# Performance work log

Measured on AMD Instinct MI355X. Metric: run time of the kernel, lower is better.

Reference implementation:

```python
import jax, jax.numpy as jnp
import numpy as np

B, S, D, H = 2, 4096, 256, 4
DH = D // H  # head dim = 64


def setup_inputs() -> dict:
    key = jax.random.key(0)
    ks = jax.random.split(key, 7)
    scale = 1.0 / np.sqrt(D)
    return {
        "x": jax.random.normal(ks[0], (B, S, D), dtype=jnp.float32),
        "Wq": jax.random.normal(ks[1], (D, D), dtype=jnp.float32) * scale,
        "bq": jax.random.normal(ks[2], (D,), dtype=jnp.float32) * scale,
        "Wk": jax.random.normal(ks[3], (D, D), dtype=jnp.float32) * scale,
        "bk": jax.random.normal(ks[4], (D,), dtype=jnp.float32) * scale,
        "Wv": jax.random.normal(ks[5], (D, D), dtype=jnp.float32) * scale,
        "bv": jax.random.normal(ks[6], (D,), dtype=jnp.float32) * scale,
    }


def reference(x, Wq, bq, Wk, bk, Wv, bv):
    b, s, d = x.shape
    # torch Linear: y = x @ W.T + b ; W stored as [out, in]
    q = (jnp.einsum('bsd,ed->bse', x, Wq) + bq).reshape(b, s, H, DH)
    k = (jnp.einsum('bsd,ed->bse', x, Wk) + bk).reshape(b, s, H, DH)
    v = (jnp.einsum('bsd,ed->bse', x, Wv) + bv).reshape(b, s, H, DH)
    # scores: [b, s(query), t(key), h]
    scores = jnp.einsum('bshd,bthd->bsth', q, k) / jnp.sqrt(jnp.float32(DH))
    # softmax over key axis t (dim=-2 in torch layout bsth)
    weights = jax.nn.softmax(scores, axis=2)
    out = jnp.einsum('bsth,bthd->bshd', weights, v)
    return out.reshape(b, s, d)
```

## Files before the change

kernel.cpp:

```cpp
#include <hip/hip_runtime.h>

#define S_LEN 4096
#define D_MODEL 256
#define NH 4
#define DH 64
#define CSC 0.18033688011112042f
#define FRAG 520

typedef __attribute__((ext_vector_type(8))) short bf16x8;
typedef __attribute__((ext_vector_type(8))) unsigned short u16x8;
typedef __attribute__((ext_vector_type(4))) float f32x4;
typedef __attribute__((ext_vector_type(16))) float f32x16;
typedef __attribute__((ext_vector_type(2))) unsigned int u32x2;
typedef __attribute__((ext_vector_type(4))) unsigned int u32x4;

#define MFMA16(a, b, c) __builtin_amdgcn_mfma_f32_16x16x32_bf16((a), (b), (c), 0, 0, 0)
#define MFMA32(a, b, c) __builtin_amdgcn_mfma_f32_32x32x16_bf16((a), (b), (c), 0, 0, 0)

static __device__ __forceinline__ unsigned short f2bf(float f) {
  unsigned int u = __float_as_uint(f);
  u += 0x7fffu + ((u >> 16) & 1u);
  return (unsigned short)(u >> 16);
}

static __device__ __forceinline__ unsigned int cvtpk(float lo, float hi) {
  unsigned int r;
  asm("v_cvt_pk_bf16_f32 %0, %1, %2" : "=v"(r) : "v"(lo), "v"(hi));
  return r;
}

static __device__ __forceinline__ u16x8 cvt8(float4 a, float4 b) {
  u16x8 v;
  v[0] = f2bf(a.x); v[1] = f2bf(a.y); v[2] = f2bf(a.z); v[3] = f2bf(a.w);
  v[4] = f2bf(b.x); v[5] = f2bf(b.y); v[6] = f2bf(b.z); v[7] = f2bf(b.w);
  return v;
}

static __device__ __forceinline__ void pack_pb(const f32x16& s0, const f32x16& s1,
                                               bf16x8* pb) {
  unsigned int u0[8], u1[8];
#pragma unroll
  for (int gg = 0; gg < 4; ++gg) {
    u0[gg * 2 + 0] = cvtpk(s0[4 * gg + 0], s0[4 * gg + 1]);
    u0[gg * 2 + 1] = cvtpk(s0[4 * gg + 2], s0[4 * gg + 3]);
    u1[gg * 2 + 0] = cvtpk(s1[4 * gg + 0], s1[4 * gg + 1]);
    u1[gg * 2 + 1] = cvtpk(s1[4 * gg + 2], s1[4 * gg + 3]);
  }
#pragma unroll
  for (int S = 0; S < 2; ++S) {
    u32x2 w0 = __builtin_amdgcn_permlane32_swap(u0[4 * S + 0], u0[4 * S + 2], false, false);
    u32x2 w1 = __builtin_amdgcn_permlane32_swap(u0[4 * S + 1], u0[4 * S + 3], false, false);
    u32x4 t0; t0[0] = w0[0]; t0[1] = w1[0]; t0[2] = w0[1]; t0[3] = w1[1];
    pb[S] = __builtin_bit_cast(bf16x8, t0);
    u32x2 w2 = __builtin_amdgcn_permlane32_swap(u1[4 * S + 0], u1[4 * S + 2], false, false);
    u32x2 w3 = __builtin_amdgcn_permlane32_swap(u1[4 * S + 1], u1[4 * S + 3], false, false);
    u32x4 t1; t1[0] = w2[0]; t1[1] = w3[0]; t1[2] = w2[1]; t1[3] = w3[1];
    pb[2 + S] = __builtin_bit_cast(bf16x8, t1);
  }
}

__global__ __launch_bounds__(256) void prep(
    const float* __restrict__ Wq, const float* __restrict__ Wk,
    const float* __restrict__ Wv, unsigned short* __restrict__ Wb)
{
  const int gid = blockIdx.x * 256 + threadIdx.x;
  const int l   = gid & 63;
  const int f   = gid >> 6;
  const int kk  = f & 7;
  const int ctn = f >> 3;
  const int ct  = ctn & 3, nt = ctn >> 2;
  const int pj  = nt >> 2, h = nt & 3;
  const float* Wsel = (pj == 0) ? Wq : (pj == 1) ? Wk : Wv;
  const float* src =
      Wsel + (size_t)(h * 64 + ct * 16 + (l & 15)) * D_MODEL + kk * 32 + (l >> 4) * 8;
  float4 a = *(const float4*)src;
  float4 b = *(const float4*)(src + 4);
  *(u16x8*)(Wb + (size_t)gid * 8) = cvt8(a, b);
}

__global__ __launch_bounds__(256) void qkv_proj(
    const float* __restrict__ x, const unsigned short* __restrict__ Wb,
    const float* __restrict__ bq, const float* __restrict__ bk,
    const float* __restrict__ bv,
    unsigned short* __restrict__ Qh, unsigned short* __restrict__ Kh,
    unsigned short* __restrict__ Vt)
{
  __shared__ unsigned short xs[32][264];
  __shared__ float tbuf[32][68];

  const int tid  = threadIdx.x;
  const int lane = tid & 63;
  const int w    = tid >> 6;
  const int r16  = lane & 15;
  const int hi   = lane >> 4;
  const int m0   = (blockIdx.x >> 2) * 32;
  const int ntB  = (blockIdx.x & 3) * 3;

  {
    const int r  = tid >> 3;
    const int c0 = (tid & 7) * 32;
    const float* xp = x + (size_t)(m0 + r) * D_MODEL + c0;
#pragma unroll
    for (int i = 0; i < 32; i += 8) {
      float4 a = *(const float4*)(xp + i);
      float4 b = *(const float4*)(xp + i + 4);
      *(u16x8*)&xs[r][c0 + i] = cvt8(a, b);
    }
  }
  __syncthreads();

  const int bb = m0 >> 12;
  const int s_base = m0 & 4095;

  for (int t = 0; t < 3; ++t) {
    const int nt = ntB + t, pj = nt >> 2, h = nt & 3;
    f32x4 acc[2] = {};
    const size_t fb = (size_t)(nt * 4 + w) * 8;
#pragma unroll
    for (int kk = 0; kk < 8; ++kk) {
      bf16x8 bw = *(const bf16x8*)(Wb + (fb + kk) * 512 + lane * 8);
#pragma unroll
      for (int rt = 0; rt < 2; ++rt) {
        bf16x8 af = *(const bf16x8*)&xs[rt * 16 + r16][kk * 32 + hi * 8];
        acc[rt] = MFMA16(af, bw, acc[rt]);
      }
    }
    const float* bsel = (pj == 0) ? bq : (pj == 1) ? bk : bv;
    const float bias = bsel[h * 64 + w * 16 + r16];
    const float scl  = (pj == 0) ? CSC : 1.0f;

#pragma unroll
    for (int rt = 0; rt < 2; ++rt)
#pragma unroll
      for (int j = 0; j < 4; ++j)
        tbuf[rt * 16 + hi * 4 + j][w * 16 + r16] = (acc[rt][j] + bias) * scl;
    __syncthreads();

    if (pj < 2) {
      const int s_l = tid >> 3, c0 = (tid & 7) * 8;
      float4 a = *(const float4*)&tbuf[s_l][c0];
      float4 b = *(const float4*)&tbuf[s_l][c0 + 4];
      unsigned short* dst = ((pj == 0) ? Qh : Kh) +
          ((size_t)(bb * NH + h) * S_LEN + s_base + s_l) * DH + c0;
      *(u16x8*)dst = cvt8(a, b);
    } else {
      const int d_l = tid & 63, sblk = (tid >> 6) * 8;
      u16x8 vv;
#pragma unroll
      for (int e = 0; e < 8; ++e) vv[e] = f2bf(tbuf[sblk + e][d_l]);
      unsigned short* dst = Vt +
          ((size_t)(bb * NH + h) * DH + d_l) * S_LEN + s_base + sblk;
      *(u16x8*)dst = vv;
    }
    __syncthreads();
  }
}

__global__ __launch_bounds__(1024) void attn(
    const unsigned short* __restrict__ Qh,
    const unsigned short* __restrict__ Kh,
    const unsigned short* __restrict__ Vt,
    float* __restrict__ out)
{
  __shared__ unsigned short KV[2][2][4][8 * FRAG];

  const int tid = threadIdx.x;
  const int ln  = tid & 63;
  const int wv  = tid >> 6;
  const int g   = wv >> 2;
  const int wq  = wv & 3;
  const int r32 = ln & 31;
  const int h   = ln >> 5;

  const int bid = blockIdx.x;
  const int bh  = bid & 7;
  const int q0  = (bid >> 3) * 128;

  const unsigned short* Qb = Qh + (size_t)bh * S_LEN * DH;
  const unsigned short* Kb = Kh + (size_t)bh * S_LEN * DH;
  const unsigned short* Vb = Vt + (size_t)bh * DH * S_LEN;

  const int q = q0 + wq * 32 + r32;
  bf16x8 qf[4];
#pragma unroll
  for (int s = 0; s < 4; ++s)
    qf[s] = *(const bf16x8*)(Qb + (size_t)q * DH + s * 16 + h * 8);

  f32x16 o0 = {}, o1 = {};
  float l_run = 0.f;

  const int u  = tid & 255;
  const int gs = tid >> 8;
  const int sr = u >> 2;
  const int sc = (u & 3) * 16;
  const int f0   = (sc >> 4) * 2 + (sr >> 5);
  const int offA = f0 * FRAG + (sr & 31) * 8;
  const int offB = offA + 256;

  uint4 kA, kB, vA, vB;
#define LOAD_CHUNK(c)                                                          \
  { const unsigned short* kp = Kb + ((size_t)(c) * 64 + sr) * DH + sc;         \
    kA = *(const uint4*)kp;  kB = *(const uint4*)(kp + 8);                     \
    const unsigned short* vp = Vb + (size_t)sr * S_LEN + (c) * 64 + sc;        \
    vA = *(const uint4*)vp;  vB = *(const uint4*)(vp + 8); }
#define STAGE(par)                                                             \
  { unsigned short* kd = &KV[par][0][gs][0];                                   \
    *(uint4*)(kd + offA) = kA;  *(uint4*)(kd + offB) = kB;                     \
    unsigned short* vd = &KV[par][1][gs][0];                                   \
    *(uint4*)(vd + offA) = vA;  *(uint4*)(vd + offB) = vB; }

  LOAD_CHUNK(gs);
  STAGE(0);
  LOAD_CHUNK(4 + gs);

  for (int it = 0; it < 16; ++it) {
    __syncthreads();
    const unsigned short* Kc = &KV[it & 1][0][g][0];
    const unsigned short* Vc = &KV[it & 1][1][g][0];
    const int lb = ln * 8;

    f32x16 s0 = {}, s1 = {};
    __builtin_amdgcn_s_setprio(1);
#pragma unroll
    for (int s = 0; s < 4; ++s) {
      bf16x8 a0 = *(const bf16x8*)(Kc + lb + (2 * s + 0) * FRAG);
      bf16x8 a1 = *(const bf16x8*)(Kc + lb + (2 * s + 1) * FRAG);
      s0 = MFMA32(a0, qf[s], s0);
      s1 = MFMA32(a1, qf[s], s1);
    }
    __builtin_amdgcn_s_setprio(0);

    float pa = 0.f, pbs = 0.f, pc = 0.f, pd = 0.f;
#pragma unroll
    for (int i = 0; i < 16; i += 2) {
      s0[i]     = __builtin_amdgcn_exp2f(s0[i]);      pa  += s0[i];
      s0[i + 1] = __builtin_amdgcn_exp2f(s0[i + 1]);  pbs += s0[i + 1];
      s1[i]     = __builtin_amdgcn_exp2f(s1[i]);      pc  += s1[i];
      s1[i + 1] = __builtin_amdgcn_exp2f(s1[i + 1]);  pd  += s1[i + 1];
    }
    l_run += (pa + pbs) + (pc + pd);

    if (it < 15) {
      STAGE((it + 1) & 1);
      int c = 4 * (it + 2) + gs;  if (c > 63) c = 63;
      LOAD_CHUNK(c);
    }

    bf16x8 pb[4];
    pack_pb(s0, s1, pb);

    __builtin_amdgcn_s_setprio(1);
#pragma unroll
    for (int s = 0; s < 4; ++s) {
      bf16x8 b0 = *(const bf16x8*)(Vc + lb + (2 * s + 0) * FRAG);
      bf16x8 b1 = *(const bf16x8*)(Vc + lb + (2 * s + 1) * FRAG);
      o0 = MFMA32(b0, pb[s], o0);
      o1 = MFMA32(b1, pb[s], o1);
    }
    __builtin_amdgcn_s_setprio(0);
  }

  __syncthreads();
  float* cb = (float*)&KV[0][0][0][0];
  const int cbase = wq * 64 + ln;

  if (g >= 2) {
    const int base = ((g - 2) * 256 + cbase) * 33;
#pragma unroll
    for (int i = 0; i < 16; ++i) { cb[base + i] = o0[i]; cb[base + 16 + i] = o1[i]; }
    cb[base + 32] = l_run;
  }
  __syncthreads();
  if (g < 2) {
    const int base = (g * 256 + cbase) * 33;
#pragma unroll
    for (int i = 0; i < 16; ++i) { o0[i] += cb[base + i]; o1[i] += cb[base + 16 + i]; }
    l_run += cb[base + 32];
  }
  __syncthreads();
  if (g == 1) {
    const int base = cbase * 33;
#pragma unroll
    for (int i = 0; i < 16; ++i) { cb[base + i] = o0[i]; cb[base + 16 + i] = o1[i]; }
    cb[base + 32] = l_run;
  }
  __syncthreads();
  if (g == 0) {
    const int base = cbase * 33;
#pragma unroll
    for (int i = 0; i < 16; ++i) { o0[i] += cb[base + i]; o1[i] += cb[base + 16 + i]; }
    l_run += cb[base + 32];

    const float lt  = l_run + __shfl_xor(l_run, 32);
    const float inv = 1.f / lt;
    const int bb = bh >> 2, hd = bh & 3;
    float* op = out + ((size_t)(bb * S_LEN + q)) * D_MODEL + hd * DH;
#pragma unroll
    for (int gg = 0; gg < 4; ++gg) {
      float4 v0, v1;
      v0.x = o0[4 * gg + 0] * inv;  v0.y = o0[4 * gg + 1] * inv;
      v0.z = o0[4 * gg + 2] * inv;  v0.w = o0[4 * gg + 3] * inv;
      *(float4*)(op + 8 * gg + 4 * h) = v0;
      v1.x = o1[4 * gg + 0] * inv;  v1.y = o1[4 * gg + 1] * inv;
      v1.z = o1[4 * gg + 2] * inv;  v1.w = o1[4 * gg + 3] * inv;
      *(float4*)(op + 32 + 8 * gg + 4 * h) = v1;
    }
  }
}

extern "C" void kernel_launch(void* const* d_in, const int* in_sizes, int n_in,
                              void* d_out, int out_size, void* d_ws, size_t ws_size,
                              hipStream_t stream) {
  const float* x  = (const float*)d_in[0];
  const float* Wq = (const float*)d_in[1];
  const float* bq = (const float*)d_in[2];
  const float* Wk = (const float*)d_in[3];
  const float* bk = (const float*)d_in[4];
  const float* Wv = (const float*)d_in[5];
  const float* bv = (const float*)d_in[6];
  float* out = (float*)d_out;

  const size_t per = (size_t)2 * NH * S_LEN * DH;
  if (ws_size < 3 * per * sizeof(unsigned short)) return;
  unsigned short* Qh = (unsigned short*)d_ws;
  unsigned short* Kh = Qh + per;
  unsigned short* Vt = Kh + per;
  unsigned short* Wb = (unsigned short*)d_out;

  prep<<<96, 256, 0, stream>>>(Wq, Wk, Wv, Wb);
  qkv_proj<<<1024, 256, 0, stream>>>(x, Wb, bq, bk, bv, Qh, Kh, Vt);
  attn<<<256, 1024, 0, stream>>>(Qh, Kh, Vt, out);
}
```

Baseline: 61.50 us.

## Software-pipeline attention loop so PV of previous chunk overlaps QK of current

Restructures the attention main loop into prologue, steady state and epilogue so each iteration issues the QK MFMAs for chunk it together with the PV MFMAs for chunk it-1. The exp2 softmax step then runs while the next chunk's matrix work can be interleaved, which is meant to hide the gap between QK and PV. It adds a second __syncthreads per iteration, because the V buffer of the previous chunk must stay valid until it is consumed. It also keeps pb live across iterations, which raises register pressure.

```diff
diff --git a/kernel.cpp b/kernel.cpp
--- a/kernel.cpp
+++ b/kernel.cpp
@@ -188,6 +188,7 @@
 
   f32x16 o0 = {}, o1 = {};
   float l_run = 0.f;
+  bf16x8 pb[4];
 
   const int u  = tid & 255;
   const int gs = tid >> 8;
@@ -212,48 +213,82 @@
   LOAD_CHUNK(gs);
   STAGE(0);
   LOAD_CHUNK(4 + gs);
-
-  for (int it = 0; it < 16; ++it) {
-    __syncthreads();
-    const unsigned short* Kc = &KV[it & 1][0][g][0];
-    const unsigned short* Vc = &KV[it & 1][1][g][0];
+  __syncthreads();
+
+  {
+    const unsigned short* Kc = &KV[0][0][g][0];
     const int lb = ln * 8;
-
-    f32x16 s0 = {}, s1 = {};
+    f32x16 t0 = {}, t1 = {};
     __builtin_amdgcn_s_setprio(1);
 #pragma unroll
     for (int s = 0; s < 4; ++s) {
       bf16x8 a0 = *(const bf16x8*)(Kc + lb + (2 * s + 0) * FRAG);
       bf16x8 a1 = *(const bf16x8*)(Kc + lb + (2 * s + 1) * FRAG);
-      s0 = MFMA32(a0, qf[s], s0);
-      s1 = MFMA32(a1, qf[s], s1);
+      t0 = MFMA32(a0, qf[s], t0);
+      t1 = MFMA32(a1, qf[s], t1);
     }
     __builtin_amdgcn_s_setprio(0);
-
+    STAGE(1);
+    LOAD_CHUNK(8 + gs);
     float pa = 0.f, pbs = 0.f, pc = 0.f, pd = 0.f;
 #pragma unroll
     for (int i = 0; i < 16; i += 2) {
-      s0[i]     = __builtin_amdgcn_exp2f(s0[i]);      pa  += s0[i];
-      s0[i + 1] = __builtin_amdgcn_exp2f(s0[i + 1]);  pbs += s0[i + 1];
-      s1[i]     = __builtin_amdgcn_exp2f(s1[i]);      pc  += s1[i];
-      s1[i + 1] = __builtin_amdgcn_exp2f(s1[i + 1]);  pd  += s1[i + 1];
+      t0[i]     = __builtin_amdgcn_exp2f(t0[i]);      pa  += t0[i];
+      t0[i + 1] = __builtin_amdgcn_exp2f(t0[i + 1]);  pbs += t0[i + 1];
+      t1[i]     = __builtin_amdgcn_exp2f(t1[i]);      pc  += t1[i];
+      t1[i + 1] = __builtin_amdgcn_exp2f(t1[i + 1]);  pd  += t1[i + 1];
     }
     l_run += (pa + pbs) + (pc + pd);
+    pack_pb(t0, t1, pb);
+  }
+
+  for (int it = 1; it < 16; ++it) {
+    __syncthreads();
+    const unsigned short* Kc = &KV[it & 1][0][g][0];
+    const unsigned short* Vp = &KV[(it - 1) & 1][1][g][0];
+    const int lb = ln * 8;
+
+    f32x16 t0 = {}, t1 = {};
+    __builtin_amdgcn_s_setprio(1);
+#pragma unroll
+    for (int s = 0; s < 4; ++s) {
+      bf16x8 a0 = *(const bf16x8*)(Kc + lb + (2 * s + 0) * FRAG);
+      bf16x8 a1 = *(const bf16x8*)(Kc + lb + (2 * s + 1) * FRAG);
+      bf16x8 b0 = *(const bf16x8*)(Vp + lb + (2 * s + 0) * FRAG);
+      bf16x8 b1 = *(const bf16x8*)(Vp + lb + (2 * s + 1) * FRAG);
+      t0 = MFMA32(a0, qf[s], t0);
+      t1 = MFMA32(a1, qf[s], t1);
+      o0 = MFMA32(b0, pb[s], o0);
+      o1 = MFMA32(b1, pb[s], o1);
+    }
+    __builtin_amdgcn_s_setprio(0);
+    __syncthreads();
 
     if (it < 15) {
       STAGE((it + 1) & 1);
       int c = 4 * (it + 2) + gs;  if (c > 63) c = 63;
       LOAD_CHUNK(c);
     }
-
-    bf16x8 pb[4];
-    pack_pb(s0, s1, pb);
-
+    float pa = 0.f, pbs = 0.f, pc = 0.f, pd = 0.f;
+#pragma unroll
+    for (int i = 0; i < 16; i += 2) {
+      t0[i]     = __builtin_amdgcn_exp2f(t0[i]);      pa  += t0[i];
+      t0[i + 1] = __builtin_amdgcn_exp2f(t0[i + 1]);  pbs += t0[i + 1];
+      t1[i]     = __builtin_amdgcn_exp2f(t1[i]);      pc  += t1[i];
+      t1[i + 1] = __builtin_amdgcn_exp2f(t1[i + 1]);  pd  += t1[i + 1];
+    }
+    l_run += (pa + pbs) + (pc + pd);
+    pack_pb(t0, t1, pb);
+  }
+
+  {
+    const unsigned short* Vp = &KV[1][1][g][0];
+    const int lb = ln * 8;
     __builtin_amdgcn_s_setprio(1);
 #pragma unroll
     for (int s = 0; s < 4; ++s) {
-      bf16x8 b0 = *(const bf16x8*)(Vc + lb + (2 * s + 0) * FRAG);
-      bf16x8 b1 = *(const bf16x8*)(Vc + lb + (2 * s + 1) * FRAG);
+      bf16x8 b0 = *(const bf16x8*)(Vp + lb + (2 * s + 0) * FRAG);
+      bf16x8 b1 = *(const bf16x8*)(Vp + lb + (2 * s + 1) * FRAG);
       o0 = MFMA32(b0, pb[s], o0);
       o1 = MFMA32(b1, pb[s], o1);
     }
```

New measurement: 71.33 us. +16.0%, slower.
